# Kernel optimization log

Hardware: AMD Instinct MI355X
Metric: run time of the kernel (lower is better)

Reference implementation:

```python
import jax, jax.numpy as jnp
import numpy as np
from math import sqrt

D_MODEL = 1024
NUM_HEADS = 16
MASK_VAL = -100000000.0


def setup_inputs() -> dict:
    key = jax.random.key(0)
    k1, k2, k3, k4, k5 = jax.random.split(key, 5)
    scale = 1.0 / sqrt(D_MODEL)
    return {
        "in_features": jax.random.normal(k1, (2, 2048, D_MODEL), dtype=jnp.float32),
        "q_proj_weight": jax.random.normal(k2, (D_MODEL, D_MODEL), dtype=jnp.float32) * scale,
        "k_proj_weight": jax.random.normal(k3, (D_MODEL, D_MODEL), dtype=jnp.float32) * scale,
        "v_proj_weight": jax.random.normal(k4, (D_MODEL, D_MODEL), dtype=jnp.float32) * scale,
        "o_proj_weight": jax.random.normal(k5, (D_MODEL, D_MODEL), dtype=jnp.float32) * scale,
    }


def _proj_heads(x, w, h):
    # x: [b, s, d_in], w: [h*d, d_in] -> [b, h, s, d]
    d = w.shape[0] // h
    w = w.reshape(h, d, w.shape[1])
    return jnp.einsum('bsi,hdi->bhsd', x, w)


def reference(in_features, q_proj_weight, k_proj_weight, v_proj_weight, o_proj_weight):
    h = NUM_HEADS
    b, s, _ = in_features.shape
    q = _proj_heads(in_features, q_proj_weight, h)  # [b,h,s,dk]
    k = _proj_heads(in_features, k_proj_weight, h)
    v = _proj_heads(in_features, v_proj_weight, h)
    d_k = q.shape[-1]
    # additive causal mask: -1e8 above diagonal
    mask = jnp.triu(jnp.full((s, s), MASK_VAL, dtype=q.dtype), k=1)[None, None]
    scores = jnp.einsum('bhqd,bhkd->bhqk', q, k) / sqrt(d_k) + mask
    attn = jax.nn.softmax(scores, axis=-1)
    out = jnp.einsum('bhqk,bhkd->bhqd', attn, v)          # [b,h,s,dv]
    out = out.transpose(0, 2, 1, 3).reshape(b, s, -1)      # [b,s,h*dv]
    return jnp.einsum('bsv,mv->bsm', out, o_proj_weight)
```

## Files before the change

kernel.cpp:

```cpp
#include <hip/hip_runtime.h>
#include <hip/hip_bf16.h>
#include <stdint.h>
#include <type_traits>

typedef __bf16 bf16;
typedef __bf16 bf16x4 __attribute__((ext_vector_type(4)));
typedef __bf16 bf16x8 __attribute__((ext_vector_type(8)));
typedef float floatx4 __attribute__((ext_vector_type(4)));
typedef unsigned int u32;

#define D_MODEL 1024
#define SEQ 2048
#define NHEADS 16
#define DH 64
#define BATCH 2
#define MROWS (BATCH * SEQ)

#define XELEMS ((size_t)MROWS * D_MODEL)
#define WELEMS ((size_t)D_MODEL * D_MODEL)
#define CVT_ELEMS (XELEMS + 4 * WELEMS)

__device__ __forceinline__ void gload_lds16(const void* g, void* l) {
  __builtin_amdgcn_global_load_lds(
      (const __attribute__((address_space(1))) u32*)g,
      (__attribute__((address_space(3))) u32*)l, 16, 0, 0);
}

__global__ __launch_bounds__(256) void cvt_f32_bf16(
    const float* __restrict__ s0, const float* __restrict__ s1,
    const float* __restrict__ s2, const float* __restrict__ s3,
    const float* __restrict__ s4, bf16* __restrict__ dst) {
  const size_t i = ((size_t)blockIdx.x * 256 + threadIdx.x) * 8;
  const float* src;
  size_t off;
  if (i < XELEMS) {
    src = s0; off = i;
  } else {
    const size_t j = i - XELEMS;
    const int r = (int)(j / WELEMS);
    src = (r == 0) ? s1 : (r == 1) ? s2 : (r == 2) ? s3 : s4;
    off = j - (size_t)r * WELEMS;
  }
  floatx4 f0 = *(const floatx4*)&src[off];
  floatx4 f1 = *(const floatx4*)&src[off + 4];
  bf16x8 o;
#pragma unroll
  for (int j = 0; j < 4; j++) { o[j] = (bf16)f0[j]; o[4 + j] = (bf16)f1[j]; }
  *(bf16x8*)&dst[i] = o;
}


__global__ __launch_bounds__(256) void gemm_qkv(
    const bf16* __restrict__ A, const bf16* __restrict__ Wq,
    const bf16* __restrict__ Wk, const bf16* __restrict__ Wv,
    bf16* __restrict__ Qo, bf16* __restrict__ Ko, bf16* __restrict__ Vto) {
  const int z = blockIdx.z;
  const bf16* W = (z == 0) ? Wq : (z == 1) ? Wk : Wv;

  __shared__ bf16 As[128 * 64];
  __shared__ bf16 Bs[128 * 64];

  const int tid = threadIdx.x;
  const int lane = tid & 63;
  const int w = tid >> 6;
  const int lo16 = lane & 15;
  const int quad = lane >> 4;
  const int wy = w >> 1, wx = w & 1;

  const int m0 = blockIdx.y * 128;
  const int n0 = blockIdx.x * 128;

  const int sl = lane >> 3;
  const int sc = ((lane & 7) ^ sl) * 8;

  const floatx4 fz = {0.f, 0.f, 0.f, 0.f};
  floatx4 acc[4][4];
#pragma unroll
  for (int i = 0; i < 4; i++)
#pragma unroll
    for (int j = 0; j < 4; j++) acc[i][j] = fz;

  auto kloop = [&](auto vt) {
    constexpr bool VT = decltype(vt)::value;
    for (int k0 = 0; k0 < 1024; k0 += 64) {
      __syncthreads();
#pragma unroll
      for (int i = 0; i < 4; i++) {
        const int seg = i * 4 + w;
        const int row = seg * 8 + sl;
        gload_lds16(&A[(size_t)(m0 + row) * 1024 + k0 + sc], &As[seg * 512]);
        gload_lds16(&W[(size_t)(n0 + row) * 1024 + k0 + sc], &Bs[seg * 512]);
      }
      __syncthreads();

#pragma unroll
      for (int kk = 0; kk < 64; kk += 32) {
        bf16x8 af[4], bfr[4];
        const int cc = (kk >> 3) + quad;
#pragma unroll
        for (int t = 0; t < 4; t++) {
          const int ra = wy * 64 + t * 16 + lo16;
          const int rb = wx * 64 + t * 16 + lo16;
          af[t]  = *(const bf16x8*)&As[ra * 64 + ((cc ^ (ra & 7)) << 3)];
          bfr[t] = *(const bf16x8*)&Bs[rb * 64 + ((cc ^ (rb & 7)) << 3)];
        }
#pragma unroll
        for (int mt = 0; mt < 4; mt++)
#pragma unroll
          for (int nt = 0; nt < 4; nt++) {
            if constexpr (VT)
              acc[mt][nt] = __builtin_amdgcn_mfma_f32_16x16x32_bf16(bfr[nt], af[mt], acc[mt][nt], 0, 0, 0);
            else
              acc[mt][nt] = __builtin_amdgcn_mfma_f32_16x16x32_bf16(af[mt], bfr[nt], acc[mt][nt], 0, 0, 0);
          }
      }
    }
  };
  if (z == 2) kloop(std::true_type{}); else kloop(std::false_type{});

  if (z < 2) {
    bf16* C = (z == 0) ? Qo : Ko;
#pragma unroll
    for (int mt = 0; mt < 4; mt++)
#pragma unroll
      for (int nt = 0; nt < 4; nt++)
#pragma unroll
        for (int r = 0; r < 4; r++) {
          const int row = m0 + wy * 64 + mt * 16 + quad * 4 + r;
          const int col = n0 + wx * 64 + nt * 16 + lo16;
          C[(size_t)row * D_MODEL + col] = (bf16)acc[mt][nt][r];
        }
  } else {
#pragma unroll
    for (int mt = 0; mt < 4; mt++)
#pragma unroll
      for (int nt = 0; nt < 4; nt++)
#pragma unroll
        for (int r = 0; r < 4; r++) {
          const int feat = n0 + wx * 64 + nt * 16 + quad * 4 + r;
          const int tok  = m0 + wy * 64 + mt * 16 + lo16;
          const int hh = feat >> 6, dd = feat & 63;
          const int bb = tok >> 11, ss = tok & 2047;
          Vto[(size_t)((bb * NHEADS + hh) * DH + dd) * SEQ + ss] = (bf16)acc[mt][nt][r];
        }
  }
}

__global__ __launch_bounds__(256) void gemm_o(
    const bf16* __restrict__ A, const bf16* __restrict__ W,
    float* __restrict__ C) {
  __shared__ bf16 As[2 * 64 * 64];
  __shared__ bf16 Bs[2 * 128 * 64];

  const int tid = threadIdx.x;
  const int lane = tid & 63;
  const int w = tid >> 6;
  const int lo16 = lane & 15;
  const int quad = lane >> 4;
  const int wy = w >> 1, wx = w & 1;

  const int m0 = blockIdx.y * 64;
  const int n0 = blockIdx.x * 128;

  const int sl = lane >> 3;
  const int sc = ((lane & 7) ^ sl) * 8;

  const floatx4 fz = {0.f, 0.f, 0.f, 0.f};
  floatx4 acc[2][4];
#pragma unroll
  for (int i = 0; i < 2; i++)
#pragma unroll
    for (int j = 0; j < 4; j++) acc[i][j] = fz;

  for (int k0 = 0; k0 < 1024; k0 += 128) {
    __syncthreads();
#pragma unroll
    for (int kh = 0; kh < 2; kh++) {
#pragma unroll
      for (int i = 0; i < 2; i++) {
        const int seg = i * 4 + w;
        const int row = seg * 8 + sl;
        gload_lds16(&A[(size_t)(m0 + row) * 1024 + k0 + kh * 64 + sc],
                    &As[kh * 4096 + seg * 512]);
      }
#pragma unroll
      for (int i = 0; i < 4; i++) {
        const int seg = i * 4 + w;
        const int row = seg * 8 + sl;
        gload_lds16(&W[(size_t)(n0 + row) * 1024 + k0 + kh * 64 + sc],
                    &Bs[kh * 8192 + seg * 512]);
      }
    }
    __syncthreads();

#pragma unroll
    for (int kk = 0; kk < 128; kk += 32) {
      const int kh = kk >> 6;
      const int cc = ((kk & 63) >> 3) + quad;
      bf16x8 af[2], bfr[4];
#pragma unroll
      for (int t = 0; t < 2; t++) {
        const int ra = wy * 32 + t * 16 + lo16;
        af[t] = *(const bf16x8*)&As[kh * 4096 + ra * 64 + ((cc ^ (ra & 7)) << 3)];
      }
#pragma unroll
      for (int t = 0; t < 4; t++) {
        const int rb = wx * 64 + t * 16 + lo16;
        bfr[t] = *(const bf16x8*)&Bs[kh * 8192 + rb * 64 + ((cc ^ (rb & 7)) << 3)];
      }
#pragma unroll
      for (int mt = 0; mt < 2; mt++)
#pragma unroll
        for (int nt = 0; nt < 4; nt++)
          acc[mt][nt] = __builtin_amdgcn_mfma_f32_16x16x32_bf16(af[mt], bfr[nt], acc[mt][nt], 0, 0, 0);
    }
  }

#pragma unroll
  for (int mt = 0; mt < 2; mt++)
#pragma unroll
    for (int nt = 0; nt < 4; nt++)
#pragma unroll
      for (int r = 0; r < 4; r++) {
        const int row = m0 + wy * 32 + mt * 16 + quad * 4 + r;
        const int col = n0 + wx * 64 + nt * 16 + lo16;
        C[(size_t)row * D_MODEL + col] = acc[mt][nt][r];
      }
}

#define LP 72

__global__ __launch_bounds__(256) void attn_causal(
    const bf16* __restrict__ Q, const bf16* __restrict__ Kg,
    const bf16* __restrict__ Vt, bf16* __restrict__ O) {
  __shared__ bf16 Ks[64 * LP];
  __shared__ bf16 VTs[64 * LP];
  __shared__ bf16 Ps[4][16 * LP];

  const int tid = threadIdx.x;
  const int lane = tid & 63;
  const int w = tid >> 6;
  const int lo16 = lane & 15;
  const int quad = lane >> 4;

  const int x = blockIdx.x;
  const int qtA = x;
  const int qtB = 31 - x;
  const int tmax = qtB;
  const int h = blockIdx.y;
  const int b = blockIdx.z;
  const size_t base  = (size_t)b * SEQ * D_MODEL + (size_t)h * DH;
  const size_t baset = (size_t)(b * NHEADS + h) * DH * SEQ;

  const int rA = qtA * 64 + w * 16 + lo16;
  const int rB = qtB * 64 + w * 16 + lo16;
  bf16x8 qfA[2], qfB[2];
#pragma unroll
  for (int ks = 0; ks < 2; ks++) {
    qfA[ks] = *(const bf16x8*)&Q[base + (size_t)rA * D_MODEL + ks * 32 + quad * 8];
    qfB[ks] = *(const bf16x8*)&Q[base + (size_t)rB * D_MODEL + ks * 32 + quad * 8];
  }

  bf16x8 onesf;
#pragma unroll
  for (int j = 0; j < 8; j++) onesf[j] = (bf16)1.0f;

  const floatx4 fz = {0.f, 0.f, 0.f, 0.f};
  floatx4 oA[4], oB[4];
  floatx4 lA = fz, lB = fz;
#pragma unroll
  for (int i = 0; i < 4; i++) { oA[i] = fz; oB[i] = fz; }

  const int kr = tid >> 3;
  const int kc = (tid & 7) * 8;

  bf16x8 kv[2], vv[2];
#pragma unroll
  for (int c = 0; c < 2; c++) {
    kv[c] = *(const bf16x8*)&Kg[base + (size_t)(c * 32 + kr) * D_MODEL + kc];
    vv[c] = *(const bf16x8*)&Vt[baset + (size_t)(c * 32 + kr) * SEQ + kc];
  }

  for (int t = 0; t <= tmax; t++) {
    const int j0 = t * 64;
    __syncthreads();
#pragma unroll
    for (int c = 0; c < 2; c++) {
      *(bf16x8*)&Ks[(c * 32 + kr) * LP + kc] = kv[c];
      *(bf16x8*)&VTs[(c * 32 + kr) * LP + kc] = vv[c];
    }
    __syncthreads();

    if (t < tmax) {
      const int j1 = j0 + 64;
#pragma unroll
      for (int c = 0; c < 2; c++) {
        kv[c] = *(const bf16x8*)&Kg[base + (size_t)(j1 + c * 32 + kr) * D_MODEL + kc];
        vv[c] = *(const bf16x8*)&Vt[baset + (size_t)(c * 32 + kr) * SEQ + j1 + kc];
      }
    }

    bf16x8 kf[4][2], vf[2][4];
#pragma unroll
    for (int nt = 0; nt < 4; nt++)
#pragma unroll
      for (int ks = 0; ks < 2; ks++)
        kf[nt][ks] = *(const bf16x8*)&Ks[(nt * 16 + lo16) * LP + ks * 32 + quad * 8];
#pragma unroll
    for (int ks = 0; ks < 2; ks++)
#pragma unroll
      for (int dt = 0; dt < 4; dt++)
        vf[ks][dt] = *(const bf16x8*)&VTs[(dt * 16 + lo16) * LP + ks * 32 + quad * 8];

    auto compute = [&](int q0s, const bf16x8* qf, floatx4* oacc, floatx4& lacc,
                       bool diag) {
      floatx4 sacc[4];
#pragma unroll
      for (int nt = 0; nt < 4; nt++) sacc[nt] = fz;
#pragma unroll
      for (int nt = 0; nt < 4; nt++)
#pragma unroll
        for (int ks = 0; ks < 2; ks++)
          sacc[nt] = __builtin_amdgcn_mfma_f32_16x16x32_bf16(kf[nt][ks], qf[ks], sacc[nt], 0, 0, 0);

      if (diag) {
        const int myq = q0s + w * 16 + lo16;
#pragma unroll
        for (int nt = 0; nt < 4; nt++) {
          const int kvb = j0 + nt * 16 + quad * 4;
          bf16x4 pk;
#pragma unroll
          for (int r = 0; r < 4; r++) {
            const float e = __builtin_amdgcn_exp2f(fmaf(sacc[nt][r], 0.18033688f, -17.3123405f));
            pk[r] = (bf16)((kvb + r > myq) ? 0.f : e);
          }
          *(bf16x4*)&Ps[w][lo16 * LP + nt * 16 + quad * 4] = pk;
        }
      } else {
#pragma unroll
        for (int nt = 0; nt < 4; nt++) {
          bf16x4 pk;
#pragma unroll
          for (int r = 0; r < 4; r++)
            pk[r] = (bf16)__builtin_amdgcn_exp2f(fmaf(sacc[nt][r], 0.18033688f, -17.3123405f));
          *(bf16x4*)&Ps[w][lo16 * LP + nt * 16 + quad * 4] = pk;
        }
      }

#pragma unroll
      for (int ks = 0; ks < 2; ks++) {
        bf16x8 pf = *(const bf16x8*)&Ps[w][lo16 * LP + ks * 32 + quad * 8];
#pragma unroll
        for (int dt = 0; dt < 4; dt++)
          oacc[dt] = __builtin_amdgcn_mfma_f32_16x16x32_bf16(pf, vf[ks][dt], oacc[dt], 0, 0, 0);
        lacc = __builtin_amdgcn_mfma_f32_16x16x32_bf16(pf, onesf, lacc, 0, 0, 0);
      }
    };

    compute(qtB * 64, qfB, oB, lB, t == qtB);
    if (t <= qtA) compute(qtA * 64, qfA, oA, lA, t == qtA);
  }

  auto finish = [&](int q0s, floatx4* oacc, floatx4 lacc) {
#pragma unroll
    for (int r = 0; r < 4; r++) {
      const float inv = 1.0f / lacc[r];
      const int row = q0s + w * 16 + quad * 4 + r;
#pragma unroll
      for (int dt = 0; dt < 4; dt++)
        O[base + (size_t)row * D_MODEL + dt * 16 + lo16] = (bf16)(oacc[dt][r] * inv);
    }
  };
  finish(qtA * 64, oA, lA);
  finish(qtB * 64, oB, lB);
}

extern "C" void kernel_launch(void* const* d_in, const int* in_sizes, int n_in,
                              void* d_out, int out_size, void* d_ws, size_t ws_size,
                              hipStream_t stream) {
  const float* X  = (const float*)d_in[0];
  const float* Wq = (const float*)d_in[1];
  const float* Wk = (const float*)d_in[2];
  const float* Wv = (const float*)d_in[3];
  const float* Wo = (const float*)d_in[4];
  float* out = (float*)d_out;

  bf16* cvt = (bf16*)d_ws;
  bf16* Xb  = cvt;
  bf16* Wqb = cvt + XELEMS;
  bf16* Wkb = Wqb + WELEMS;
  bf16* Wvb = Wkb + WELEMS;
  bf16* Wob = Wvb + WELEMS;
  bf16* Qb  = cvt + CVT_ELEMS;
  bf16* Kb  = Qb + XELEMS;
  bf16* Vtb = Kb + XELEMS;
  bf16* Ob  = Vtb + XELEMS;

  dim3 blk(256);
  cvt_f32_bf16<<<dim3((u32)(CVT_ELEMS / (256 * 8))), blk, 0, stream>>>(
      X, Wq, Wk, Wv, Wo, cvt);
  gemm_qkv<<<dim3(8, 32, 3), blk, 0, stream>>>(Xb, Wqb, Wkb, Wvb, Qb, Kb, Vtb);
  attn_causal<<<dim3(16, NHEADS, BATCH), blk, 0, stream>>>(Qb, Kb, Vtb, Ob);
  gemm_o<<<dim3(8, 64), blk, 0, stream>>>(Ob, Wob, out);
}
```

Measured before the change: 180.9 us.

## Split attention KV tile across two wave groups with LDS reduction

Doubles the attention block to 512 threads. Two groups of four waves each process half of every 64-key tile (32 keys) for the same query rows, and the partial O and row sums are combined through shared memory at the end. The aim is more waves per block to hide latency, given that the grid has only 512 blocks. In exchange it adds a final LDS reduction, a larger shared footprint and duplicated Q loads. It also relies on the unnormalized exp softmax with a fixed offset, which makes the partial sums additive.

```diff
diff --git a/kernel.cpp b/kernel.cpp
--- a/kernel.cpp
+++ b/kernel.cpp
@@ -230,16 +230,19 @@
 
 #define LP 72
 
-__global__ __launch_bounds__(256) void attn_causal(
+__global__ __launch_bounds__(512) void attn_causal(
     const bf16* __restrict__ Q, const bf16* __restrict__ Kg,
     const bf16* __restrict__ Vt, bf16* __restrict__ O) {
   __shared__ bf16 Ks[64 * LP];
   __shared__ bf16 VTs[64 * LP];
-  __shared__ bf16 Ps[4][16 * LP];
+  __shared__ bf16 Ps[8][16 * LP];
+  __shared__ float Es[4][64][40];
 
   const int tid = threadIdx.x;
   const int lane = tid & 63;
-  const int w = tid >> 6;
+  const int wid = tid >> 6;
+  const int g = wid >> 2;
+  const int w4 = wid & 3;
   const int lo16 = lane & 15;
   const int quad = lane >> 4;
 
@@ -252,8 +255,8 @@
   const size_t base  = (size_t)b * SEQ * D_MODEL + (size_t)h * DH;
   const size_t baset = (size_t)(b * NHEADS + h) * DH * SEQ;
 
-  const int rA = qtA * 64 + w * 16 + lo16;
-  const int rB = qtB * 64 + w * 16 + lo16;
+  const int rA = qtA * 64 + w4 * 16 + lo16;
+  const int rB = qtB * 64 + w4 * 16 + lo16;
   bf16x8 qfA[2], qfB[2];
 #pragma unroll
   for (int ks = 0; ks < 2; ks++) {
@@ -274,105 +277,117 @@
   const int kr = tid >> 3;
   const int kc = (tid & 7) * 8;
 
-  bf16x8 kv[2], vv[2];
-#pragma unroll
-  for (int c = 0; c < 2; c++) {
-    kv[c] = *(const bf16x8*)&Kg[base + (size_t)(c * 32 + kr) * D_MODEL + kc];
-    vv[c] = *(const bf16x8*)&Vt[baset + (size_t)(c * 32 + kr) * SEQ + kc];
-  }
+  bf16x8 kv, vv;
+  kv = *(const bf16x8*)&Kg[base + (size_t)kr * D_MODEL + kc];
+  vv = *(const bf16x8*)&Vt[baset + (size_t)kr * SEQ + kc];
 
   for (int t = 0; t <= tmax; t++) {
     const int j0 = t * 64;
     __syncthreads();
-#pragma unroll
-    for (int c = 0; c < 2; c++) {
-      *(bf16x8*)&Ks[(c * 32 + kr) * LP + kc] = kv[c];
-      *(bf16x8*)&VTs[(c * 32 + kr) * LP + kc] = vv[c];
-    }
+    *(bf16x8*)&Ks[kr * LP + kc] = kv;
+    *(bf16x8*)&VTs[kr * LP + kc] = vv;
     __syncthreads();
 
     if (t < tmax) {
       const int j1 = j0 + 64;
-#pragma unroll
-      for (int c = 0; c < 2; c++) {
-        kv[c] = *(const bf16x8*)&Kg[base + (size_t)(j1 + c * 32 + kr) * D_MODEL + kc];
-        vv[c] = *(const bf16x8*)&Vt[baset + (size_t)(c * 32 + kr) * SEQ + j1 + kc];
-      }
+      kv = *(const bf16x8*)&Kg[base + (size_t)(j1 + kr) * D_MODEL + kc];
+      vv = *(const bf16x8*)&Vt[baset + (size_t)kr * SEQ + j1 + kc];
     }
 
-    bf16x8 kf[4][2], vf[2][4];
-#pragma unroll
-    for (int nt = 0; nt < 4; nt++)
+    bf16x8 kf[2][2], vf[4];
+#pragma unroll
+    for (int n = 0; n < 2; n++)
 #pragma unroll
       for (int ks = 0; ks < 2; ks++)
-        kf[nt][ks] = *(const bf16x8*)&Ks[(nt * 16 + lo16) * LP + ks * 32 + quad * 8];
-#pragma unroll
-    for (int ks = 0; ks < 2; ks++)
-#pragma unroll
-      for (int dt = 0; dt < 4; dt++)
-        vf[ks][dt] = *(const bf16x8*)&VTs[(dt * 16 + lo16) * LP + ks * 32 + quad * 8];
+        kf[n][ks] = *(const bf16x8*)&Ks[((2 * g + n) * 16 + lo16) * LP + ks * 32 + quad * 8];
+#pragma unroll
+    for (int dt = 0; dt < 4; dt++)
+      vf[dt] = *(const bf16x8*)&VTs[(dt * 16 + lo16) * LP + g * 32 + quad * 8];
 
     auto compute = [&](int q0s, const bf16x8* qf, floatx4* oacc, floatx4& lacc,
                        bool diag) {
-      floatx4 sacc[4];
-#pragma unroll
-      for (int nt = 0; nt < 4; nt++) sacc[nt] = fz;
-#pragma unroll
-      for (int nt = 0; nt < 4; nt++)
+      floatx4 sacc[2];
+#pragma unroll
+      for (int n = 0; n < 2; n++) sacc[n] = fz;
+#pragma unroll
+      for (int n = 0; n < 2; n++)
 #pragma unroll
         for (int ks = 0; ks < 2; ks++)
-          sacc[nt] = __builtin_amdgcn_mfma_f32_16x16x32_bf16(kf[nt][ks], qf[ks], sacc[nt], 0, 0, 0);
+          sacc[n] = __builtin_amdgcn_mfma_f32_16x16x32_bf16(kf[n][ks], qf[ks], sacc[n], 0, 0, 0);
 
       if (diag) {
-        const int myq = q0s + w * 16 + lo16;
-#pragma unroll
-        for (int nt = 0; nt < 4; nt++) {
-          const int kvb = j0 + nt * 16 + quad * 4;
+        const int myq = q0s + w4 * 16 + lo16;
+#pragma unroll
+        for (int n = 0; n < 2; n++) {
+          const int kvb = j0 + (2 * g + n) * 16 + quad * 4;
           bf16x4 pk;
 #pragma unroll
           for (int r = 0; r < 4; r++) {
-            const float e = __builtin_amdgcn_exp2f(fmaf(sacc[nt][r], 0.18033688f, -17.3123405f));
+            const float e = __builtin_amdgcn_exp2f(fmaf(sacc[n][r], 0.18033688f, -17.3123405f));
             pk[r] = (bf16)((kvb + r > myq) ? 0.f : e);
           }
-          *(bf16x4*)&Ps[w][lo16 * LP + nt * 16 + quad * 4] = pk;
+          *(bf16x4*)&Ps[wid][lo16 * LP + n * 16 + quad * 4] = pk;
         }
       } else {
 #pragma unroll
-        for (int nt = 0; nt < 4; nt++) {
+        for (int n = 0; n < 2; n++) {
           bf16x4 pk;
 #pragma unroll
           for (int r = 0; r < 4; r++)
-            pk[r] = (bf16)__builtin_amdgcn_exp2f(fmaf(sacc[nt][r], 0.18033688f, -17.3123405f));
-          *(bf16x4*)&Ps[w][lo16 * LP + nt * 16 + quad * 4] = pk;
+            pk[r] = (bf16)__builtin_amdgcn_exp2f(fmaf(sacc[n][r], 0.18033688f, -17.3123405f));
+          *(bf16x4*)&Ps[wid][lo16 * LP + n * 16 + quad * 4] = pk;
         }
       }
 
-#pragma unroll
-      for (int ks = 0; ks < 2; ks++) {
-        bf16x8 pf = *(const bf16x8*)&Ps[w][lo16 * LP + ks * 32 + quad * 8];
-#pragma unroll
-        for (int dt = 0; dt < 4; dt++)
-          oacc[dt] = __builtin_amdgcn_mfma_f32_16x16x32_bf16(pf, vf[ks][dt], oacc[dt], 0, 0, 0);
-        lacc = __builtin_amdgcn_mfma_f32_16x16x32_bf16(pf, onesf, lacc, 0, 0, 0);
-      }
+      bf16x8 pf = *(const bf16x8*)&Ps[wid][lo16 * LP + quad * 8];
+#pragma unroll
+      for (int dt = 0; dt < 4; dt++)
+        oacc[dt] = __builtin_amdgcn_mfma_f32_16x16x32_bf16(pf, vf[dt], oacc[dt], 0, 0, 0);
+      lacc = __builtin_amdgcn_mfma_f32_16x16x32_bf16(pf, onesf, lacc, 0, 0, 0);
     };
 
     compute(qtB * 64, qfB, oB, lB, t == qtB);
     if (t <= qtA) compute(qtA * 64, qfA, oA, lA, t == qtA);
   }
 
-  auto finish = [&](int q0s, floatx4* oacc, floatx4 lacc) {
-#pragma unroll
-    for (int r = 0; r < 4; r++) {
-      const float inv = 1.0f / lacc[r];
-      const int row = q0s + w * 16 + quad * 4 + r;
-#pragma unroll
-      for (int dt = 0; dt < 4; dt++)
-        O[base + (size_t)row * D_MODEL + dt * 16 + lo16] = (bf16)(oacc[dt][r] * inv);
-    }
-  };
-  finish(qtA * 64, oA, lA);
-  finish(qtB * 64, oB, lB);
+  if (g == 1) {
+    float* e = Es[w4][lane];
+#pragma unroll
+    for (int dt = 0; dt < 4; dt++)
+#pragma unroll
+      for (int r = 0; r < 4; r++) e[dt * 4 + r] = oA[dt][r];
+#pragma unroll
+    for (int r = 0; r < 4; r++) e[16 + r] = lA[r];
+#pragma unroll
+    for (int dt = 0; dt < 4; dt++)
+#pragma unroll
+      for (int r = 0; r < 4; r++) e[20 + dt * 4 + r] = oB[dt][r];
+#pragma unroll
+    for (int r = 0; r < 4; r++) e[36 + r] = lB[r];
+  }
+  __syncthreads();
+  if (g == 0) {
+    const float* e = Es[w4][lane];
+#pragma unroll
+    for (int dt = 0; dt < 4; dt++)
+#pragma unroll
+      for (int r = 0; r < 4; r++) { oA[dt][r] += e[dt * 4 + r]; oB[dt][r] += e[20 + dt * 4 + r]; }
+#pragma unroll
+    for (int r = 0; r < 4; r++) { lA[r] += e[16 + r]; lB[r] += e[36 + r]; }
+
+    auto finish = [&](int q0s, floatx4* oacc, floatx4 lacc) {
+#pragma unroll
+      for (int r = 0; r < 4; r++) {
+        const float inv = 1.0f / lacc[r];
+        const int row = q0s + w4 * 16 + quad * 4 + r;
+#pragma unroll
+        for (int dt = 0; dt < 4; dt++)
+          O[base + (size_t)row * D_MODEL + dt * 16 + lo16] = (bf16)(oacc[dt][r] * inv);
+      }
+    };
+    finish(qtA * 64, oA, lA);
+    finish(qtB * 64, oB, lB);
+  }
 }
 
 extern "C" void kernel_launch(void* const* d_in, const int* in_sizes, int n_in,
@@ -400,6 +415,6 @@
   cvt_f32_bf16<<<dim3((u32)(CVT_ELEMS / (256 * 8))), blk, 0, stream>>>(
       X, Wq, Wk, Wv, Wo, cvt);
   gemm_qkv<<<dim3(8, 32, 3), blk, 0, stream>>>(Xb, Wqb, Wkb, Wvb, Qb, Kb, Vtb);
-  attn_causal<<<dim3(16, NHEADS, BATCH), blk, 0, stream>>>(Qb, Kb, Vtb, Ob);
+  attn_causal<<<dim3(16, NHEADS, BATCH), dim3(512), 0, stream>>>(Qb, Kb, Vtb, Ob);
   gemm_o<<<dim3(8, 64), blk, 0, stream>>>(Ob, Wob, out);
 }
```

Result: no change. 179.5 us (-0.8%).
